# Kernel optimization log

Hardware: AMD Instinct MI355X
Metric: run time of the kernel (lower is better)

## Reference

```python
import jax, jax.numpy as jnp
import numpy as np

TOP_K = 2

def setup_inputs() -> dict:
    key = jax.random.key(0)
    ks = jax.random.split(key, 5)
    B, S, D, E, R, H = 4, 2048, 1024, 8, 128, 4096
    s = 0.02
    return {
        "hidden_states": jax.random.normal(ks[0], (B, S, D), jnp.float32),
        "w_route": jax.random.normal(ks[1], (E, D, R), jnp.float32) * s,
        "w3": jax.random.normal(ks[2], (E, D, H), jnp.float32) * s,
        "wr2h": jax.random.normal(ks[3], (E, R, H), jnp.float32) * s,
        "wh2d": jax.random.normal(ks[4], (E, H, D), jnp.float32) * s,
    }

def reference(hidden_states, w_route, w3, wr2h, wh2d):
    B, S, D = hidden_states.shape
    E = w_route.shape[0]
    x = hidden_states.reshape(-1, D)                      # [N, D]
    N = x.shape[0]
    # per-expert routing activations (also reused as w1_state inside experts)
    acts = jnp.einsum('nd,edr->ner', x, w_route)          # [N, E, R]
    norms = jnp.linalg.norm(acts, axis=-1)                # [N, E] router logits
    probs = jax.nn.softmax(norms.astype(jnp.float32), axis=-1)
    topw, sel = jax.lax.top_k(probs, TOP_K)               # [N, k]
    topw = topw / topw.sum(axis=-1, keepdims=True)
    topw = topw.astype(x.dtype)
    # dense combine weights: routing weight if expert selected, else 0
    combine = jnp.zeros((N, E), x.dtype).at[jnp.arange(N)[:, None], sel].add(topw)
    out = jnp.zeros_like(x)
    for e in range(E):  # fixed small expert count
        h = (x @ w3[e]) * jax.nn.silu(acts[:, e, :] @ wr2h[e])  # [N, H]
        out = out + (h @ wh2d[e]) * combine[:, e:e + 1]
    final = out.reshape(B, S, D)
    # load balancing loss on the router logits (expert_act_norms)
    mask = jax.nn.one_hot(sel, E, dtype=jnp.float32)      # [N, k, E]
    tokens_per_expert = mask.mean(axis=0)                 # [k, E]
    router_prob_per_expert = probs.mean(axis=0)           # [E]
    bl_loss = jnp.sum(tokens_per_expert * router_prob_per_expert[None, :]) * E
    return final, norms, bl_loss
```

## Files before the change

kernel.cpp:

```cpp
#include <hip/hip_runtime.h>


#define DEV static __device__ __forceinline__

typedef float  f32x4  __attribute__((ext_vector_type(4)));
typedef __bf16 bf16x8 __attribute__((ext_vector_type(8)));

DEV unsigned short f2bf(float f) {
  union { float f; unsigned u; } v; v.f = f;
  unsigned r = v.u + 0x7fffu + ((v.u >> 16) & 1u);
  return (unsigned short)(r >> 16);
}
DEV float bf2f(unsigned short b) {
  union { unsigned u; float f; } v; v.u = ((unsigned)b) << 16;
  return v.f;
}

DEV void gll16(const void* g, void* l) {
  __builtin_amdgcn_global_load_lds(
      (const __attribute__((address_space(1))) unsigned int*)g,
      (__attribute__((address_space(3))) unsigned int*)l, 16, 0, 0);
}

DEV f32x4 mfma16(bf16x8 a, bf16x8 b, f32x4 c) {
  return __builtin_amdgcn_mfma_f32_16x16x32_bf16(a, b, c, 0, 0, 0);
}

DEV int xcd_swz_gen(int bid, int nwg) {
  int x = bid & 7, o = bid >> 3;
  int q = nwg >> 3, r = nwg & 7;
  return (x < r ? x * (q + 1) : r * (q + 1) + (x - r) * q) + o;
}

DEV bf16x8 frag_read(const unsigned short* lds, int row, int kb) {
  int off = row * 128 + ((kb * 2) ^ ((row & 7) << 4));
  return *(const bf16x8*)((const char*)lds + off);
}
DEV void stage_linear(const unsigned short* base, size_t pitch, int k0,
                      unsigned short* lds, int tid) {
  int wq = tid >> 6, lane = tid & 63;
#pragma unroll
  for (int i = 0; i < 4; ++i) {
    int s = wq * 256 + i * 64 + lane;
    int row = s >> 3, b = s & 7;
    int bb = b ^ (row & 7);
    const unsigned short* g = base + (size_t)row * pitch + (size_t)(k0 + bb * 8);
    gll16(g, lds + (size_t)(wq * 256 + i * 64) * 8);
  }
}
DEV void stage_gather(const unsigned short* base, size_t pitch, size_t colOff,
                      int k0, const int* toks, unsigned short* lds, int tid) {
  int wq = tid >> 6, lane = tid & 63;
#pragma unroll
  for (int i = 0; i < 4; ++i) {
    int s = wq * 256 + i * 64 + lane;
    int row = s >> 3, b = s & 7;
    int bb = b ^ (row & 7);
    const unsigned short* g =
        base + (size_t)toks[row] * pitch + colOff + (size_t)(k0 + bb * 8);
    gll16(g, lds + (size_t)(wq * 256 + i * 64) * 8);
  }
}
DEV void mfma_block(const unsigned short* A, const unsigned short* B,
                    f32x4 (&acc)[4][4], int wm, int wn, int lg, int lc) {
#pragma unroll
  for (int ks = 0; ks < 2; ++ks) {
    int kb = ks * 32 + lg * 8;
    bf16x8 af[4], bff[4];
#pragma unroll
    for (int i = 0; i < 4; ++i) {
      af[i]  = frag_read(A, wm * 64 + i * 16 + lc, kb);
      bff[i] = frag_read(B, wn * 64 + i * 16 + lc, kb);
    }
#pragma unroll
    for (int mf = 0; mf < 4; ++mf)
#pragma unroll
      for (int nf = 0; nf < 4; ++nf)
        acc[mf][nf] = mfma16(af[mf], bff[nf], acc[mf][nf]);
  }
}


__global__ __launch_bounds__(256) void k_cast_x(const float* __restrict__ x,
    unsigned short* __restrict__ xh, unsigned short* __restrict__ xl) {
  int stride = gridDim.x * blockDim.x;
  for (int i = blockIdx.x * blockDim.x + threadIdx.x; i < 8192 * 1024 / 4;
       i += stride) {
    float4 v = ((const float4*)x)[i];
    ushort4 h, l;
    h.x = f2bf(v.x); l.x = f2bf(v.x - bf2f(h.x));
    h.y = f2bf(v.y); l.y = f2bf(v.y - bf2f(h.y));
    h.z = f2bf(v.z); l.z = f2bf(v.z - bf2f(h.z));
    h.w = f2bf(v.w); l.w = f2bf(v.w - bf2f(h.w));
    ((ushort4*)xh)[i] = h;
    ((ushort4*)xl)[i] = l;
  }
}

__global__ void k_zero(int* cnt, float* probsum) {
  int t = threadIdx.x;
  if (t < 16) cnt[t] = 0;
  if (t < 8)  probsum[t] = 0.f;
}

__global__ __launch_bounds__(256) void k_transp(const float* __restrict__ src,
    unsigned short* __restrict__ dst, int K, int N) {
  int ntn = N >> 6;
  int kt = blockIdx.x / ntn, nt = blockIdx.x % ntn;
  int e = blockIdx.y;
  __shared__ float tl[64][65];
  const float* s = src + (size_t)e * K * N;
  unsigned short* d = dst + (size_t)e * N * K;
  int tid = threadIdx.x;
  int c4 = (tid & 15) * 4, rr = tid >> 4;
#pragma unroll
  for (int p = 0; p < 4; ++p) {
    int row = rr + p * 16;
    float4 v = *(const float4*)(s + (size_t)(kt * 64 + row) * N + nt * 64 + c4);
    tl[row][c4] = v.x; tl[row][c4 + 1] = v.y;
    tl[row][c4 + 2] = v.z; tl[row][c4 + 3] = v.w;
  }
  __syncthreads();
#pragma unroll
  for (int p = 0; p < 4; ++p) {
    int n = rr + p * 16;
    ushort4 o;
    o.x = f2bf(tl[c4 + 0][n]); o.y = f2bf(tl[c4 + 1][n]);
    o.z = f2bf(tl[c4 + 2][n]); o.w = f2bf(tl[c4 + 3][n]);
    *(ushort4*)(d + (size_t)(nt * 64 + n) * K + kt * 64 + c4) = o;
  }
}

__global__ __launch_bounds__(256) void k_transp_split(const float* __restrict__ src,
    unsigned short* __restrict__ dh, unsigned short* __restrict__ dl, int K, int N) {
  int ntn = N >> 6;
  int kt = blockIdx.x / ntn, nt = blockIdx.x % ntn;
  int e = blockIdx.y;
  __shared__ float tl[64][65];
  const float* s = src + (size_t)e * K * N;
  size_t dbase = (size_t)e * N * K;
  int tid = threadIdx.x;
  int c4 = (tid & 15) * 4, rr = tid >> 4;
#pragma unroll
  for (int p = 0; p < 4; ++p) {
    int row = rr + p * 16;
    float4 v = *(const float4*)(s + (size_t)(kt * 64 + row) * N + nt * 64 + c4);
    tl[row][c4] = v.x; tl[row][c4 + 1] = v.y;
    tl[row][c4 + 2] = v.z; tl[row][c4 + 3] = v.w;
  }
  __syncthreads();
#pragma unroll
  for (int p = 0; p < 4; ++p) {
    int n = rr + p * 16;
    ushort4 oh, ol;
#pragma unroll
    for (int i = 0; i < 4; ++i) {
      float v = tl[c4 + i][n];
      unsigned short hh = f2bf(v);
      unsigned short ll = f2bf(v - bf2f(hh));
      ((unsigned short*)&oh)[i] = hh;
      ((unsigned short*)&ol)[i] = ll;
    }
    *(ushort4*)(dh + dbase + (size_t)(nt * 64 + n) * K + kt * 64 + c4) = oh;
    *(ushort4*)(dl + dbase + (size_t)(nt * 64 + n) * K + kt * 64 + c4) = ol;
  }
}

__global__ __launch_bounds__(256) void k_route_gemm(
    const unsigned short* __restrict__ xh, const unsigned short* __restrict__ xl,
    const unsigned short* __restrict__ wrh_t, const unsigned short* __restrict__ wrl_t,
    unsigned short* __restrict__ acts, float* __restrict__ norms_out) {
  __shared__ __align__(16) unsigned short Ah[128 * 64], Al[128 * 64];
  __shared__ __align__(16) unsigned short Bh[128 * 64], Bl[128 * 64];
  __shared__ float ssq_s[128][2];
  int tid = threadIdx.x;
  int mt = blockIdx.x, e = blockIdx.y;
  int wq = tid >> 6, lane = tid & 63;
  int wm = wq >> 1, wn = wq & 1, lg = lane >> 4, lc = lane & 15;
  f32x4 acc[4][4] = {};
  const unsigned short* ah_src = xh + (size_t)mt * 128 * 1024;
  const unsigned short* al_src = xl + (size_t)mt * 128 * 1024;
  const unsigned short* bh_src = wrh_t + (size_t)e * 128 * 1024;
  const unsigned short* bl_src = wrl_t + (size_t)e * 128 * 1024;
  for (int kt = 0; kt < 16; ++kt) {
    int k0 = kt * 64;
    stage_linear(ah_src, 1024, k0, Ah, tid);
    stage_linear(al_src, 1024, k0, Al, tid);
    stage_linear(bh_src, 1024, k0, Bh, tid);
    stage_linear(bl_src, 1024, k0, Bl, tid);
    __syncthreads();
#pragma unroll
    for (int ks = 0; ks < 2; ++ks) {
      int kb = ks * 32 + lg * 8;
      bf16x8 ahf[4], alf[4], bhf[4], blf[4];
#pragma unroll
      for (int i = 0; i < 4; ++i) {
        ahf[i] = frag_read(Ah, wm * 64 + i * 16 + lc, kb);
        alf[i] = frag_read(Al, wm * 64 + i * 16 + lc, kb);
        bhf[i] = frag_read(Bh, wn * 64 + i * 16 + lc, kb);
        blf[i] = frag_read(Bl, wn * 64 + i * 16 + lc, kb);
      }
#pragma unroll
      for (int mf = 0; mf < 4; ++mf)
#pragma unroll
        for (int nf = 0; nf < 4; ++nf) {
          acc[mf][nf] = mfma16(ahf[mf], bhf[nf], acc[mf][nf]);
          acc[mf][nf] = mfma16(alf[mf], bhf[nf], acc[mf][nf]);
          acc[mf][nf] = mfma16(ahf[mf], blf[nf], acc[mf][nf]);
        }
    }
    __syncthreads();
  }
  float ssq[4][4];
#pragma unroll
  for (int mf = 0; mf < 4; ++mf)
#pragma unroll
    for (int r = 0; r < 4; ++r) ssq[mf][r] = 0.f;
#pragma unroll
  for (int mf = 0; mf < 4; ++mf)
#pragma unroll
    for (int nf = 0; nf < 4; ++nf)
#pragma unroll
      for (int r = 0; r < 4; ++r) {
        float v = acc[mf][nf][r];
        int row = wm * 64 + mf * 16 + lg * 4 + r;
        int col = wn * 64 + nf * 16 + lc;
        acts[(size_t)(mt * 128 + row) * 1024 + e * 128 + col] = f2bf(v);
        ssq[mf][r] += v * v;
      }
#pragma unroll
  for (int mf = 0; mf < 4; ++mf)
#pragma unroll
    for (int r = 0; r < 4; ++r) {
      float s = ssq[mf][r];
      s += __shfl_xor(s, 1); s += __shfl_xor(s, 2);
      s += __shfl_xor(s, 4); s += __shfl_xor(s, 8);
      if (lc == 0) ssq_s[wm * 64 + mf * 16 + lg * 4 + r][wn] = s;
    }
  __syncthreads();
  if (tid < 128) {
    float s = ssq_s[tid][0] + ssq_s[tid][1];
    norms_out[(size_t)(mt * 128 + tid) * 8 + e] = sqrtf(s);
  }
}

__global__ __launch_bounds__(256) void k_router(const float* __restrict__ norms,
    float* __restrict__ topw, int* __restrict__ sel,
    int* __restrict__ cnt, float* __restrict__ probsum) {
  __shared__ float ps_s[8];
  __shared__ int cnt_s[16];
  int tid = threadIdx.x;
  if (tid < 8)  ps_s[tid] = 0.f;
  if (tid < 16) cnt_s[tid] = 0;
  __syncthreads();
  int n = blockIdx.x * 256 + tid;
  float p[8], mx = -3.4e38f;
#pragma unroll
  for (int e = 0; e < 8; ++e) { p[e] = norms[(size_t)n * 8 + e]; mx = fmaxf(mx, p[e]); }
  float s = 0.f;
#pragma unroll
  for (int e = 0; e < 8; ++e) { p[e] = __expf(p[e] - mx); s += p[e]; }
  float inv = 1.f / s;
  int i1 = 0; float v1 = p[0];
#pragma unroll
  for (int e = 1; e < 8; ++e) if (p[e] > v1) { v1 = p[e]; i1 = e; }
  int i2 = -1; float v2 = -1.f;
#pragma unroll
  for (int e = 0; e < 8; ++e) if (e != i1 && p[e] > v2) { v2 = p[e]; i2 = e; }
  float wsum = v1 + v2;
  topw[n * 2 + 0] = v1 / wsum;
  topw[n * 2 + 1] = v2 / wsum;
  sel[n * 2 + 0] = i1;
  sel[n * 2 + 1] = i2;
  atomicAdd(&cnt_s[i1], 1);
  atomicAdd(&cnt_s[8 + i2], 1);
#pragma unroll
  for (int e = 0; e < 8; ++e) atomicAdd(&ps_s[e], p[e] * inv);
  __syncthreads();
  if (tid < 8)  atomicAdd(&probsum[tid], ps_s[tid]);
  if (tid < 16) atomicAdd(&cnt[tid], cnt_s[tid]);
}

__global__ void k_plan(const int* __restrict__ cnt, const float* __restrict__ probsum,
                       int* __restrict__ offs, int* __restrict__ fill,
                       int4* __restrict__ tilemap, float* __restrict__ bl_out) {
  int t = 0;
  for (int k = 0; k < 2; ++k) {
    int pos = 0;
    for (int e = 0; e < 8; ++e) {
      int c = cnt[k * 8 + e];
      offs[k * 8 + e] = pos;
      int ntl = (c + 127) >> 7;
      for (int i = 0; i < ntl; ++i) {
        int rr = c - i * 128; if (rr > 128) rr = 128;
        tilemap[t] = make_int4(e, k * 8192 + pos + i * 128, rr, 0);
        ++t;
      }
      pos += c;
    }
  }
  for (; t < 160; ++t) tilemap[t] = make_int4(0, 0, 0, 0);
  for (int i = 0; i < 16; ++i) fill[i] = 0;
  float bl = 0.f;
  for (int e = 0; e < 8; ++e)
    bl += ((float)(cnt[e] + cnt[8 + e]) / 8192.f) * (probsum[e] / 8192.f);
  *bl_out = bl * 8.f;
}

__global__ __launch_bounds__(256) void k_fill(const int* __restrict__ sel,
    const float* __restrict__ topw, const int* __restrict__ offs,
    int* __restrict__ fill, int* __restrict__ list01, float* __restrict__ wlist) {
  int n = blockIdx.x * 256 + threadIdx.x;
#pragma unroll
  for (int k = 0; k < 2; ++k) {
    int e = sel[n * 2 + k];
    int pos = atomicAdd(&fill[k * 8 + e], 1);
    int idx = k * 8192 + offs[k * 8 + e] + pos;
    list01[idx] = n;
    wlist[idx] = topw[n * 2 + k];
  }
}

__global__ __launch_bounds__(256) void k_gemm1(
    const unsigned short* __restrict__ xh, const unsigned short* __restrict__ acts,
    const unsigned short* __restrict__ w3t, const unsigned short* __restrict__ wr2h_t,
    const int* __restrict__ list, const int4* __restrict__ tilemap, int tile_lo,
    int nt, unsigned short* __restrict__ hbuf) {
  __shared__ __align__(16) unsigned short A[128 * 64], B[128 * 64];
  __shared__ int toks[128];
  int wg = xcd_swz_gen((int)blockIdx.x, nt * 32);
  int tloc = wg >> 5, bn = wg & 31;
  int4 ent = tilemap[tile_lo + tloc];
  int e = ent.x, posbase = ent.y, rows = ent.z;
  if (rows == 0) return;
  int tid = threadIdx.x;
  if (tid < 128) {
    int rr = tid < rows ? tid : rows - 1;
    toks[tid] = list[posbase + rr];
  }
  __syncthreads();
  int wq = tid >> 6, lane = tid & 63;
  int wm = wq >> 1, wn = wq & 1, lg = lane >> 4, lc = lane & 15;
  f32x4 acc_a[4][4] = {};
  const unsigned short* bsrc = w3t + ((size_t)e * 4096 + bn * 128) * 1024;
  for (int kt = 0; kt < 16; ++kt) {
    int k0 = kt * 64;
    stage_gather(xh, 1024, 0, k0, toks, A, tid);
    stage_linear(bsrc, 1024, k0, B, tid);
    __syncthreads();
    mfma_block(A, B, acc_a, wm, wn, lg, lc);
    __syncthreads();
  }
  f32x4 acc_s[4][4] = {};
  const unsigned short* b2src = wr2h_t + ((size_t)e * 4096 + bn * 128) * 128;
  for (int kt = 0; kt < 2; ++kt) {
    int k0 = kt * 64;
    stage_gather(acts, 1024, (size_t)e * 128, k0, toks, A, tid);
    stage_linear(b2src, 128, k0, B, tid);
    __syncthreads();
    mfma_block(A, B, acc_s, wm, wn, lg, lc);
    __syncthreads();
  }
  size_t hrow0 = (size_t)tloc * 128;
#pragma unroll
  for (int mf = 0; mf < 4; ++mf)
#pragma unroll
    for (int nf = 0; nf < 4; ++nf)
#pragma unroll
      for (int r = 0; r < 4; ++r) {
        int row = wm * 64 + mf * 16 + lg * 4 + r;
        if (row < rows) {
          int col = wn * 64 + nf * 16 + lc;
          float sv = acc_s[mf][nf][r];
          float hv = acc_a[mf][nf][r] * (sv / (1.f + __expf(-sv)));
          hbuf[(hrow0 + row) * 4096 + (size_t)bn * 128 + col] = f2bf(hv);
        }
      }
}

__global__ __launch_bounds__(256) void k_gemm2(
    const unsigned short* __restrict__ hbuf, const unsigned short* __restrict__ wh2dt,
    const int* __restrict__ list, const float* __restrict__ wlist,
    const int4* __restrict__ tilemap, int tile_lo, int nt,
    float* __restrict__ out) {
  __shared__ __align__(16) unsigned short A[128 * 64], B[128 * 64];
  __shared__ int toks[128];
  __shared__ float wr_s[128];
  int wg = xcd_swz_gen((int)blockIdx.x, nt * 16);
  int tloc = wg >> 4, bn = (wg >> 1) & 7, ks = wg & 1;
  int4 ent = tilemap[tile_lo + tloc];
  int e = ent.x, posbase = ent.y, rows = ent.z;
  if (rows == 0) return;
  int tid = threadIdx.x;
  if (tid < 128) {
    int rr = tid < rows ? tid : rows - 1;
    toks[tid] = list[posbase + rr];
    wr_s[tid] = wlist[posbase + rr];
  }
  __syncthreads();
  int wq = tid >> 6, lane = tid & 63;
  int wm = wq >> 1, wn = wq & 1, lg = lane >> 4, lc = lane & 15;
  f32x4 acc[4][4] = {};
  const unsigned short* asrc = hbuf + (size_t)tloc * 128 * 4096;
  const unsigned short* bsrc = wh2dt + ((size_t)e * 1024 + bn * 128) * 4096;
  int kbase = ks * 2048;
  for (int kt = 0; kt < 32; ++kt) {
    int k0 = kbase + kt * 64;
    stage_linear(asrc, 4096, k0, A, tid);
    stage_linear(bsrc, 4096, k0, B, tid);
    __syncthreads();
    mfma_block(A, B, acc, wm, wn, lg, lc);
    __syncthreads();
  }
#pragma unroll
  for (int mf = 0; mf < 4; ++mf)
#pragma unroll
    for (int nf = 0; nf < 4; ++nf)
#pragma unroll
      for (int r = 0; r < 4; ++r) {
        int row = wm * 64 + mf * 16 + lg * 4 + r;
        if (row < rows) {
          int col = wn * 64 + nf * 16 + lc;
          float v = acc[mf][nf][r] * wr_s[row];
          atomicAdd(out + (size_t)toks[row] * 1024 + bn * 128 + col, v);
        }
      }
}


extern "C" void kernel_launch(void* const* d_in, const int* in_sizes, int n_in,
                              void* d_out, int out_size, void* d_ws, size_t ws_size,
                              hipStream_t stream) {
  (void)in_sizes; (void)n_in; (void)out_size;
  const float* x      = (const float*)d_in[0];
  const float* wroute = (const float*)d_in[1];
  const float* w3     = (const float*)d_in[2];
  const float* wr2h   = (const float*)d_in[3];
  const float* wh2d   = (const float*)d_in[4];
  float* out = (float*)d_out;

  char* ws = (char*)d_ws;
  size_t off = 0;
  auto carve = [&](size_t bytes) -> void* {
    void* p = ws + off; off += (bytes + 255) & ~(size_t)255; return p;
  };
  unsigned short* xh     = (unsigned short*)carve((size_t)8192 * 1024 * 2);
  unsigned short* xl     = (unsigned short*)carve((size_t)8192 * 1024 * 2);
  unsigned short* wrh_t  = (unsigned short*)carve((size_t)8 * 128 * 1024 * 2);
  unsigned short* wrl_t  = (unsigned short*)carve((size_t)8 * 128 * 1024 * 2);
  unsigned short* w3t    = (unsigned short*)carve((size_t)8 * 4096 * 1024 * 2);
  unsigned short* wr2h_t = (unsigned short*)carve((size_t)8 * 4096 * 128 * 2);
  unsigned short* wh2dt  = (unsigned short*)carve((size_t)8 * 1024 * 4096 * 2);
  unsigned short* acts   = (unsigned short*)carve((size_t)8192 * 1024 * 2);
  int*   list01 = (int*)carve(2 * 8192 * 4);
  float* wlist  = (float*)carve(2 * 8192 * 4);
  int*   sel    = (int*)carve(8192 * 2 * 4);
  float* topw   = (float*)carve(8192 * 2 * 4);
  int*   ctr    = (int*)carve(8192);
  int* cnt = ctr; int* fill = ctr + 16; int* offs = ctr + 32;
  float* probsum = (float*)(ctr + 48);
  int4* tilemap = (int4*)(ctr + 64);

  size_t avail = ws_size > off ? ws_size - off : 0;
  int tpc = 0;
  const int cands[4] = {160, 80, 40, 20};
  for (int i = 0; i < 4; ++i) {
    if ((size_t)cands[i] * 128 * 4096 * 2 <= avail) { tpc = cands[i]; break; }
  }
  if (!tpc) return;
  unsigned short* hbuf = (unsigned short*)(ws + off);

  float* norms_out = out + 8388608;
  float* bl_out    = out + 8454144;

  hipMemsetAsync(out, 0, (size_t)8388608 * 4, stream);
  k_cast_x<<<2048, 256, 0, stream>>>(x, xh, xl);
  k_zero<<<1, 64, 0, stream>>>(cnt, probsum);
  k_transp<<<dim3(16 * 64, 8), 256, 0, stream>>>(w3, w3t, 1024, 4096);
  k_transp<<<dim3(64 * 16, 8), 256, 0, stream>>>(wh2d, wh2dt, 4096, 1024);
  k_transp<<<dim3(2 * 64, 8), 256, 0, stream>>>(wr2h, wr2h_t, 128, 4096);
  k_transp_split<<<dim3(16 * 2, 8), 256, 0, stream>>>(wroute, wrh_t, wrl_t, 1024, 128);
  k_route_gemm<<<dim3(64, 8), 256, 0, stream>>>(xh, xl, wrh_t, wrl_t, acts, norms_out);
  k_router<<<32, 256, 0, stream>>>(norms_out, topw, sel, cnt, probsum);
  k_plan<<<1, 1, 0, stream>>>(cnt, probsum, offs, fill, tilemap, bl_out);
  k_fill<<<32, 256, 0, stream>>>(sel, topw, offs, fill, list01, wlist);

  int nchunk = (160 + tpc - 1) / tpc;
  for (int c = 0; c < nchunk; ++c) {
    int tile_lo = c * tpc;
    int nt = 160 - tile_lo < tpc ? 160 - tile_lo : tpc;
    k_gemm1<<<nt * 32, 256, 0, stream>>>(
        xh, acts, w3t, wr2h_t, list01, tilemap, tile_lo, nt, hbuf);
    k_gemm2<<<nt * 16, 256, 0, stream>>>(
        hbuf, wh2dt, list01, wlist, tilemap, tile_lo, nt, out);
  }
}
```

Baseline: 841.5 us.

## Use 256x256 tiles with double-buffered async LDS pipeline in second expert GEMM

The second expert GEMM moves from 128x128 tiles with 256 threads to 256x256 tiles with 512 threads. Tiles are loaded through global_load_lds into a double-buffered, XOR-swizzled LDS layout, and MFMA phases are interleaved with prefetch under explicit waitcnt, barriers and priority hints. The planner now builds a 256-row tile map plus a derived 128-row map so gemm1 keeps its old tiling. The goal is more data reuse per tile and hiding of global load latency, at the cost of heavy LDS use, 512-thread occupancy limits, and relying on tpc being even.

```diff
diff --git a/kernel.cpp b/kernel.cpp
--- a/kernel.cpp
+++ b/kernel.cpp
@@ -5,6 +5,9 @@
 
 typedef float  f32x4  __attribute__((ext_vector_type(4)));
 typedef __bf16 bf16x8 __attribute__((ext_vector_type(8)));
+
+#define VMCNT_(n) asm volatile("s_waitcnt vmcnt(" #n ")" ::: "memory")
+#define VMCNT(n) VMCNT_(n)
 
 DEV unsigned short f2bf(float f) {
   union { float f; unsigned u; } v; v.f = f;
@@ -284,22 +287,32 @@
 __global__ void k_plan(const int* __restrict__ cnt, const float* __restrict__ probsum,
                        int* __restrict__ offs, int* __restrict__ fill,
                        int4* __restrict__ tilemap, float* __restrict__ bl_out) {
+  int4* map256 = tilemap;
+  int4* map128 = tilemap + 80;
   int t = 0;
   for (int k = 0; k < 2; ++k) {
     int pos = 0;
     for (int e = 0; e < 8; ++e) {
       int c = cnt[k * 8 + e];
       offs[k * 8 + e] = pos;
-      int ntl = (c + 127) >> 7;
+      int ntl = (c + 255) >> 8;
       for (int i = 0; i < ntl; ++i) {
-        int rr = c - i * 128; if (rr > 128) rr = 128;
-        tilemap[t] = make_int4(e, k * 8192 + pos + i * 128, rr, 0);
+        int rr = c - i * 256; if (rr > 256) rr = 256;
+        map256[t] = make_int4(e, k * 8192 + pos + i * 256, rr, 0);
         ++t;
       }
       pos += c;
     }
   }
-  for (; t < 160; ++t) tilemap[t] = make_int4(0, 0, 0, 0);
+  for (; t < 80; ++t) map256[t] = make_int4(0, 0, 0, 0);
+  for (int i = 0; i < 80; ++i) {
+    int4 m = map256[i];
+    for (int h = 0; h < 2; ++h) {
+      int r = m.z - h * 128;
+      if (r < 0) r = 0; if (r > 128) r = 128;
+      map128[i * 2 + h] = make_int4(m.x, m.y + h * 128, r, 0);
+    }
+  }
   for (int i = 0; i < 16; ++i) fill[i] = 0;
   float bl = 0.f;
   for (int e = 0; e < 8; ++e)
@@ -378,53 +391,144 @@
       }
 }
 
-__global__ __launch_bounds__(256) void k_gemm2(
+__global__ __launch_bounds__(512, 2) void k_gemm2(
     const unsigned short* __restrict__ hbuf, const unsigned short* __restrict__ wh2dt,
     const int* __restrict__ list, const float* __restrict__ wlist,
-    const int4* __restrict__ tilemap, int tile_lo, int nt,
+    const int4* __restrict__ map256, int tile_lo, int nt,
     float* __restrict__ out) {
-  __shared__ __align__(16) unsigned short A[128 * 64], B[128 * 64];
-  __shared__ int toks[128];
-  __shared__ float wr_s[128];
-  int wg = xcd_swz_gen((int)blockIdx.x, nt * 16);
-  int tloc = wg >> 4, bn = (wg >> 1) & 7, ks = wg & 1;
-  int4 ent = tilemap[tile_lo + tloc];
+  __shared__ __align__(16) unsigned short SA[2][256 * 64];
+  __shared__ __align__(16) unsigned short SB[2][256 * 64];
+  __shared__ int toks[256];
+  __shared__ float wr_s[256];
+  int wg = xcd_swz_gen((int)blockIdx.x, nt * 8);
+  int tloc = wg >> 3, bn = (wg >> 1) & 3, ks = wg & 1;
+  int4 ent = map256[tile_lo + tloc];
   int e = ent.x, posbase = ent.y, rows = ent.z;
   if (rows == 0) return;
   int tid = threadIdx.x;
-  if (tid < 128) {
+  if (tid < 256) {
     int rr = tid < rows ? tid : rows - 1;
     toks[tid] = list[posbase + rr];
     wr_s[tid] = wlist[posbase + rr];
   }
   __syncthreads();
   int wq = tid >> 6, lane = tid & 63;
-  int wm = wq >> 1, wn = wq & 1, lg = lane >> 4, lc = lane & 15;
-  f32x4 acc[4][4] = {};
-  const unsigned short* asrc = hbuf + (size_t)tloc * 128 * 4096;
-  const unsigned short* bsrc = wh2dt + ((size_t)e * 1024 + bn * 128) * 4096;
+  int wm = wq >> 2, wn = wq & 3, lg = lane >> 4, lc = lane & 15;
   int kbase = ks * 2048;
-  for (int kt = 0; kt < 32; ++kt) {
-    int k0 = kbase + kt * 64;
-    stage_linear(asrc, 4096, k0, A, tid);
-    stage_linear(bsrc, 4096, k0, B, tid);
-    __syncthreads();
-    mfma_block(A, B, acc, wm, wn, lg, lc);
-    __syncthreads();
-  }
-#pragma unroll
-  for (int mf = 0; mf < 4; ++mf)
-#pragma unroll
-    for (int nf = 0; nf < 4; ++nf)
-#pragma unroll
-      for (int r = 0; r < 4; ++r) {
-        int row = wm * 64 + mf * 16 + lg * 4 + r;
-        if (row < rows) {
-          int col = wn * 64 + nf * 16 + lc;
-          float v = acc[mf][nf][r] * wr_s[row];
-          atomicAdd(out + (size_t)toks[row] * 1024 + bn * 128 + col, v);
-        }
-      }
+
+  int s0 = tid, s1 = tid + 512;
+  int r0 = s0 >> 3, c0 = ((s0 & 7) ^ (r0 & 7)) * 8;
+  int r1 = s1 >> 3, c1 = ((s1 & 7) ^ (r1 & 7)) * 8;
+  const unsigned short* a0 = hbuf + ((size_t)tloc * 256 + r0) * 4096 + kbase + c0;
+  const unsigned short* a1 = hbuf + ((size_t)tloc * 256 + r1) * 4096 + kbase + c1;
+  const unsigned short* b0 =
+      wh2dt + ((size_t)e * 1024 + bn * 256 + r0) * 4096 + kbase + c0;
+  const unsigned short* b1 =
+      wh2dt + ((size_t)e * 1024 + bn * 256 + r1) * 4096 + kbase + c1;
+
+  auto stA = [&](int kt, int h, int bi) {
+    size_t ho = (size_t)h * 128 * 4096;
+    gll16(a0 + ho + kt * 64, &SA[bi][(size_t)(h * 1024 + s0) * 8]);
+    gll16(a1 + ho + kt * 64, &SA[bi][(size_t)(h * 1024 + s1) * 8]);
+  };
+  auto stB = [&](int kt, int h, int bi) {
+    size_t ho = (size_t)h * 128 * 4096;
+    gll16(b0 + ho + kt * 64, &SB[bi][(size_t)(h * 1024 + s0) * 8]);
+    gll16(b1 + ho + kt * 64, &SB[bi][(size_t)(h * 1024 + s1) * 8]);
+  };
+
+  f32x4 acc[2][4][2][2] = {};
+  bf16x8 af[4][2], bf[2][2][2];
+
+#define RA(BI, QM)                                                           \
+  _Pragma("unroll") for (int mf = 0; mf < 4; ++mf)                           \
+  _Pragma("unroll") for (int k2 = 0; k2 < 2; ++k2)                           \
+    af[mf][k2] = frag_read(SA[BI], wm * 128 + QM * 64 + mf * 16 + lc,        \
+                           k2 * 32 + lg * 8);
+#define RB(BI, QN)                                                           \
+  _Pragma("unroll") for (int nf = 0; nf < 2; ++nf)                           \
+  _Pragma("unroll") for (int k2 = 0; k2 < 2; ++k2)                           \
+    bf[QN][nf][k2] = frag_read(SB[BI], wn * 64 + QN * 32 + nf * 16 + lc,     \
+                               k2 * 32 + lg * 8);
+#define PH_MMA(QM, QN)                                                       \
+  __builtin_amdgcn_sched_barrier(0);                                         \
+  __builtin_amdgcn_s_barrier();                                              \
+  asm volatile("s_waitcnt lgkmcnt(0)" ::: "memory");                         \
+  __builtin_amdgcn_sched_barrier(0);                                         \
+  __builtin_amdgcn_s_setprio(1);                                             \
+  _Pragma("unroll") for (int mf = 0; mf < 4; ++mf)                           \
+  _Pragma("unroll") for (int nf = 0; nf < 2; ++nf)                           \
+  _Pragma("unroll") for (int k2 = 0; k2 < 2; ++k2)                           \
+    acc[QM][mf][QN][nf] =                                                    \
+        mfma16(af[mf][k2], bf[QN][nf][k2], acc[QM][mf][QN][nf]);             \
+  __builtin_amdgcn_s_setprio(0);                                             \
+  __builtin_amdgcn_sched_barrier(0);                                         \
+  __builtin_amdgcn_s_barrier();
+
+  stA(0, 0, 0); stA(0, 1, 0); stB(0, 0, 0); stB(0, 1, 0);
+  stB(1, 0, 1); stB(1, 1, 1);
+  VMCNT(4);
+  __builtin_amdgcn_s_barrier();
+
+  for (int it = 0; it < 15; ++it) {
+    int u = 2 * it;
+    RA(0, 0); RB(0, 0); stA(u + 1, 0, 1);
+    PH_MMA(0, 0);
+    RB(0, 1); stA(u + 1, 1, 1);
+    PH_MMA(0, 1);
+    RA(0, 1); stB(u + 2, 0, 0);
+    PH_MMA(1, 1);
+    stB(u + 2, 1, 0);
+    VMCNT(4);
+    PH_MMA(1, 0);
+    RA(1, 0); RB(1, 0); stA(u + 2, 0, 0);
+    PH_MMA(0, 0);
+    RB(1, 1); stA(u + 2, 1, 0);
+    PH_MMA(0, 1);
+    RA(1, 1); stB(u + 3, 0, 1);
+    PH_MMA(1, 1);
+    stB(u + 3, 1, 1);
+    VMCNT(4);
+    PH_MMA(1, 0);
+  }
+  {
+    RA(0, 0); RB(0, 0); stA(31, 0, 1);
+    PH_MMA(0, 0);
+    RB(0, 1); stA(31, 1, 1);
+    PH_MMA(0, 1);
+    RA(0, 1);
+    PH_MMA(1, 1);
+    VMCNT(0);
+    PH_MMA(1, 0);
+    RA(1, 0); RB(1, 0);
+    PH_MMA(0, 0);
+    RB(1, 1);
+    PH_MMA(0, 1);
+    RA(1, 1);
+    PH_MMA(1, 1);
+    PH_MMA(1, 0);
+  }
+#undef RA
+#undef RB
+#undef PH_MMA
+
+#pragma unroll
+  for (int qm = 0; qm < 2; ++qm)
+#pragma unroll
+    for (int mf = 0; mf < 4; ++mf)
+#pragma unroll
+      for (int qn = 0; qn < 2; ++qn)
+#pragma unroll
+        for (int nf = 0; nf < 2; ++nf)
+#pragma unroll
+          for (int r = 0; r < 4; ++r) {
+            int row = wm * 128 + qm * 64 + mf * 16 + lg * 4 + r;
+            if (row < rows) {
+              int col = wn * 64 + qn * 32 + nf * 16 + lc;
+              float v = acc[qm][mf][qn][nf][r] * wr_s[row];
+              atomicAdd(out + (size_t)toks[row] * 1024 + bn * 256 + col, v);
+            }
+          }
 }
 
 
@@ -490,8 +594,8 @@
     int tile_lo = c * tpc;
     int nt = 160 - tile_lo < tpc ? 160 - tile_lo : tpc;
     k_gemm1<<<nt * 32, 256, 0, stream>>>(
-        xh, acts, w3t, wr2h_t, list01, tilemap, tile_lo, nt, hbuf);
-    k_gemm2<<<nt * 16, 256, 0, stream>>>(
-        hbuf, wh2dt, list01, wlist, tilemap, tile_lo, nt, out);
-  }
-}
+        xh, acts, w3t, wr2h_t, list01, tilemap + 80, tile_lo, nt, hbuf);
+    k_gemm2<<<(nt / 2) * 8, 512, 0, stream>>>(
+        hbuf, wh2dt, list01, wlist, tilemap, tile_lo / 2, nt / 2, out);
+  }
+}
```

Result: faster. 802.8 us (-4.6%).
